# Kernel optimization log

Hardware: AMD Instinct MI355X
Metric: run time of the kernel (lower is better)

Reference implementation:

```python
import jax, jax.numpy as jnp
import numpy as np

NEG = 0.01  # leaky_relu negative slope used throughout AttentiveFP


def _seg_softmax(logits, seg, num):
    # softmax over entries grouped by segment id (PyG softmax w/ 1e-16 eps)
    m = jax.ops.segment_max(logits, seg, num_segments=num)
    m = jnp.where(jnp.isfinite(m), m, 0.0)
    e = jnp.exp(logits - m[seg])
    s = jax.ops.segment_sum(e, seg, num_segments=num)
    return e / (s[seg] + 1e-16)


def _gru(x, h, wi, wh, bi, bh):
    # torch.nn.GRUCell math
    gi = x @ wi.T + bi
    gh = h @ wh.T + bh
    ir, iz, inn = jnp.split(gi, 3, axis=-1)
    hr, hz, hn = jnp.split(gh, 3, axis=-1)
    r = jax.nn.sigmoid(ir + hr)
    z = jax.nn.sigmoid(iz + hz)
    n = jnp.tanh(inn + r * hn)
    return (1.0 - z) * n + z * h


def _forward(x, edge_attr, mol_feats, lin1_w, lin1_b, gate_lin1_w, gate_lin2_w, gate_att_l, gate_att_r, gate_bias, grus_wi, grus_wh, grus_bi, grus_bh, atom_w, atom_att_src, atom_att_dst, atom_bias, mol_w, mol_att_src, mol_att_dst, mol_bias, lin2_w, lin2_b, fcm0_w, fcm0_b, fcm1_w, fcm1_b, fcm2_w, fcm2_b, fc0_w, fc0_b, fc1_w, fc1_b, fc2_w, fc2_b, fc3_w, fc3_b, fc4_w, fc4_b, edge_index, batch):
    N = x.shape[0]
    G = mol_feats.shape[0]
    src, dst = edge_index[0], edge_index[1]
    lrelu = lambda v: jax.nn.leaky_relu(v, NEG)
    # AttentiveFP (eval mode: dropout off)
    xh = lrelu(x @ lin1_w.T + lin1_b)  # [N,H]
    # --- GATEConv: edge-conditioned attention, add aggregation ---
    m = lrelu(jnp.concatenate([xh[src], edge_attr], axis=-1) @ gate_lin1_w.T)  # [E,H]
    a = lrelu(m @ gate_att_l + (xh @ gate_att_r)[dst])
    a = _seg_softmax(a, dst, N)
    h = jax.ops.segment_sum((m @ gate_lin2_w.T) * a[:, None], dst, num_segments=N) + gate_bias
    xh = jax.nn.relu(_gru(jax.nn.elu(h), xh, grus_wi[0], grus_wh[0], grus_bi[0], grus_bh[0]))
    # --- GATConv layers (num_layers-1 = 2, heads=1, no self loops) ---
    for l in range(2):
        xl = xh @ atom_w[l].T
        a = lrelu((xl @ atom_att_src[l])[src] + (xl @ atom_att_dst[l])[dst])
        a = _seg_softmax(a, dst, N)
        h = jax.ops.segment_sum(xl[src] * a[:, None], dst, num_segments=N) + atom_bias[l]
        xh = jax.nn.relu(_gru(jax.nn.elu(h), xh, grus_wi[1 + l], grus_wh[1 + l], grus_bi[1 + l], grus_bh[1 + l]))
    # --- attentive graph readout (num_timesteps = 3) ---
    out = jax.nn.relu(jax.ops.segment_sum(xh, batch, num_segments=G))  # [G,H]
    xm = xh @ mol_w.T            # atom-side lin (x fixed across timesteps)
    a_src = xm @ mol_att_src
    for _ in range(3):
        a = lrelu(a_src + ((out @ mol_w.T) @ mol_att_dst)[batch])
        a = _seg_softmax(a, batch, G)
        h = jax.ops.segment_sum(xm * a[:, None], batch, num_segments=G) + mol_bias
        out = jax.nn.relu(_gru(jax.nn.elu(h), out, grus_wi[3], grus_wh[3], grus_bi[3], grus_bh[3]))
    hg = out @ lin2_w.T + lin2_b  # [G,256]
    # --- mol-feature MLP branch (SiLU) ---
    hm = jax.nn.silu(mol_feats @ fcm0_w.T + fcm0_b)
    hm = jax.nn.silu(hm @ fcm1_w.T + fcm1_b)
    hm = jax.nn.silu(hm @ fcm2_w.T + fcm2_b)
    # --- fusion MLP ---
    hg = jnp.concatenate([hg, hm], axis=1)  # [G,512]
    hg = jax.nn.silu(hg @ fc0_w.T + fc0_b)
    hg = jax.nn.silu(hg @ fc1_w.T + fc1_b)
    hg = jax.nn.silu(hg @ fc2_w.T + fc2_b)
    hg = jax.nn.silu(hg @ fc3_w.T + fc3_b)
    return hg @ fc4_w.T + fc4_b  # [G,1]


def setup_inputs() -> dict:
    key = jax.random.key(0)
    ks = iter(jax.random.split(key, 64))
    def W(*shape):
        return jax.random.normal(next(ks), shape, jnp.float32) / np.float32(np.sqrt(shape[-1]))
    def B(*shape):
        return 0.02 * jax.random.normal(next(ks), shape, jnp.float32)
    N, E, G = 131072, 262144, 8192
    Fn, Fe, Fm, H = 64, 16, 200, 256
    return dict(
        x=jax.random.normal(next(ks), (N, Fn), jnp.float32),
        edge_attr=jax.random.normal(next(ks), (E, Fe), jnp.float32),
        mol_feats=jax.random.normal(next(ks), (G, Fm), jnp.float32),
        lin1_w=W(H, Fn), lin1_b=B(H),
        gate_lin1_w=W(H, H + Fe), gate_lin2_w=W(H, H),
        gate_att_l=W(H), gate_att_r=W(H), gate_bias=B(H),
        grus_wi=W(4, 3 * H, H), grus_wh=W(4, 3 * H, H), grus_bi=B(4, 3 * H), grus_bh=B(4, 3 * H),
        atom_w=W(2, H, H), atom_att_src=W(2, H), atom_att_dst=W(2, H), atom_bias=B(2, H),
        mol_w=W(H, H), mol_att_src=W(H), mol_att_dst=W(H), mol_bias=B(H),
        lin2_w=W(H, H), lin2_b=B(H),
        fcm0_w=W(H, Fm), fcm0_b=B(H), fcm1_w=W(H, H), fcm1_b=B(H), fcm2_w=W(H, H), fcm2_b=B(H),
        fc0_w=W(512, 512), fc0_b=B(512), fc1_w=W(512, 512), fc1_b=B(512),
        fc2_w=W(512, 512), fc2_b=B(512), fc3_w=W(128, 512), fc3_b=B(128),
        fc4_w=W(1, 128), fc4_b=B(1),
        edge_index=jax.random.randint(next(ks), (2, E), 0, N),
        batch=jnp.sort(jax.random.randint(next(ks), (N,), 0, G)),
    )


def reference(x, edge_attr, mol_feats, lin1_w, lin1_b, gate_lin1_w, gate_lin2_w, gate_att_l, gate_att_r, gate_bias, grus_wi, grus_wh, grus_bi, grus_bh, atom_w, atom_att_src, atom_att_dst, atom_bias, mol_w, mol_att_src, mol_att_dst, mol_bias, lin2_w, lin2_b, fcm0_w, fcm0_b, fcm1_w, fcm1_b, fcm2_w, fcm2_b, fc0_w, fc0_b, fc1_w, fc1_b, fc2_w, fc2_b, fc3_w, fc3_b, fc4_w, fc4_b, edge_index, batch):
    return _forward(x, edge_attr, mol_feats, lin1_w, lin1_b, gate_lin1_w, gate_lin2_w, gate_att_l, gate_att_r, gate_bias, grus_wi, grus_wh, grus_bi, grus_bh, atom_w, atom_att_src, atom_att_dst, atom_bias, mol_w, mol_att_src, mol_att_dst, mol_bias, lin2_w, lin2_b, fcm0_w, fcm0_b, fcm1_w, fcm1_b, fcm2_w, fcm2_b, fc0_w, fc0_b, fc1_w, fc1_b, fc2_w, fc2_b, fc3_w, fc3_b, fc4_w, fc4_b, edge_index, batch)
```

## Files before the change

### kernel.cpp

```cpp
#include <hip/hip_runtime.h>
#include <hip/hip_bf16.h>
#include <math.h>


typedef unsigned short u16;
typedef u16 u16x8 __attribute__((ext_vector_type(8)));
typedef short s16x8 __attribute__((ext_vector_type(8)));
typedef float f32x4 __attribute__((ext_vector_type(4)));

__device__ __forceinline__ float u2f(u16 u) { return __uint_as_float(((unsigned)u) << 16); }
__device__ __forceinline__ u16 f2u(float f) {
    return __builtin_bit_cast(u16, __float2bfloat16(f));
}

#define NEGS 0.01f

typedef const __attribute__((address_space(1))) unsigned gas1_t;
typedef __attribute__((address_space(3))) unsigned las3_t;
__device__ __forceinline__ void gload16(const void* g, void* l) {
    __builtin_amdgcn_global_load_lds((gas1_t*)g, (las3_t*)l, 16, 0, 0);
}

__device__ __forceinline__ unsigned fkey(float f) {
    unsigned u = __float_as_uint(f);
    return (u & 0x80000000u) ? ~u : (u | 0x80000000u);
}
__device__ __forceinline__ float funkey(unsigned k) {
    return (k & 0x80000000u) ? __uint_as_float(k ^ 0x80000000u) : __uint_as_float(~k);
}
#define KEY_NEG_INF 0x007FFFFFu

static inline int cdiv(int a, int b) { return (a + b - 1) / b; }

__global__ void fill_f32(float* p, float v, size_t n) {
    size_t i = (size_t)blockIdx.x * 256 + threadIdx.x;
    if (i < n) p[i] = v;
}
__global__ void fill_u32(unsigned* p, unsigned v, int n) {
    int i = blockIdx.x * 256 + threadIdx.x;
    if (i < n) p[i] = v;
}
__global__ void copy_f2b(const float* s, u16* d, size_t n) {
    size_t i = (size_t)blockIdx.x * 256 + threadIdx.x;
    if (i < n) d[i] = f2u(s[i]);
}
__global__ void matvecT_k(const float* W, const float* a, float* v, int K, int Jout) {
    int j = blockIdx.x * 256 + threadIdx.x;
    if (j >= Jout) return;
    float s = 0.f;
    for (int k = 0; k < K; k++) s += W[(size_t)k * Jout + j] * a[k];
    v[j] = s;
}
__global__ void edge_add_lrelu(float* elog, const float* r, const int* dsti, int E) {
    int i = blockIdx.x * 256 + threadIdx.x;
    if (i < E) {
        float v = elog[i] + r[dsti[i]];
        elog[i] = v > 0.f ? v : NEGS * v;
    }
}
__global__ void pair_logit(float* elog, const float* s, const float* d,
                           const int* srci, const int* dsti, int E) {
    int i = blockIdx.x * 256 + threadIdx.x;
    if (i < E) {
        float v = s[srci[i]] + d[dsti[i]];
        elog[i] = v > 0.f ? v : NEGS * v;
    }
}
__global__ void node_logit(float* nlog, const float* asrc, const float* wg,
                           const int* batch, int N) {
    int i = blockIdx.x * 256 + threadIdx.x;
    if (i < N) {
        float v = asrc[i] + wg[batch[i]];
        nlog[i] = v > 0.f ? v : NEGS * v;
    }
}
__global__ void seg_max_k(const float* logit, const int* idx, unsigned* key, int n) {
    int i = blockIdx.x * 256 + threadIdx.x;
    if (i < n) atomicMax(&key[idx[i]], fkey(logit[i]));
}
__global__ void seg_exp_k(const float* logit, const int* idx, const unsigned* key,
                          float* ex, float* sum, int n) {
    int i = blockIdx.x * 256 + threadIdx.x;
    if (i < n) {
        float e = expf(logit[i] - funkey(key[idx[i]]));
        ex[i] = e;
        atomicAdd(&sum[idx[i]], e);
    }
}
__global__ void seg_div_k(const float* ex, const int* idx, const float* sum,
                          float* a, int n) {
    int i = blockIdx.x * 256 + threadIdx.x;
    if (i < n) a[i] = ex[i] / (sum[idx[i]] + 1e-16f);
}
__global__ void rowdot2_b(const u16* X, const float* v1, const float* v2,
                          float* o1, float* o2, int M) {
    int r = blockIdx.x * 4 + (threadIdx.x >> 6);
    int lane = threadIdx.x & 63;
    if (r >= M) return;
    const u16* row = X + (size_t)r * 256 + lane * 4;
    float p1 = 0.f, p2 = 0.f;
#pragma unroll
    for (int q = 0; q < 4; q++) {
        float xv = u2f(row[q]);
        p1 += xv * v1[lane * 4 + q];
        if (v2) p2 += xv * v2[lane * 4 + q];
    }
    for (int off = 32; off; off >>= 1) {
        p1 += __shfl_down(p1, off);
        if (v2) p2 += __shfl_down(p2, off);
    }
    if (lane == 0) {
        o1[r] = p1;
        if (v2) o2[r] = p2;
    }
}
__global__ void rowdot_f(const float* X, const float* v1, float* o1, int M) {
    int r = blockIdx.x * 4 + (threadIdx.x >> 6);
    int lane = threadIdx.x & 63;
    if (r >= M) return;
    float4 a = ((const float4*)(X + (size_t)r * 256))[lane];
    float4 b = ((const float4*)v1)[lane];
    float p1 = a.x * b.x + a.y * b.y + a.z * b.z + a.w * b.w;
    for (int off = 32; off; off >>= 1) p1 += __shfl_down(p1, off);
    if (lane == 0) o1[r] = p1;
}
__global__ void fc4_k(const float* X, const float* w, const float* b, float* out, int G) {
    int g = blockIdx.x * 4 + (threadIdx.x >> 6);
    int lane = threadIdx.x & 63;
    if (g >= G) return;
    float2 xv = ((const float2*)(X + (size_t)g * 128))[lane];
    float2 wv = ((const float2*)w)[lane];
    float p = xv.x * wv.x + xv.y * wv.y;
    for (int off = 32; off; off >>= 1) p += __shfl_down(p, off);
    if (lane == 0) out[g] = p + b[0];
}

__global__ void count_dst(const int* dst, int* cnt, int E) {
    int i = blockIdx.x * 256 + threadIdx.x;
    if (i < E) atomicAdd(&cnt[dst[i]], 1);
}
__global__ void scan1(const int* cnt, int* part, int N) {
    __shared__ int sm[256];
    int i = blockIdx.x * 256 + threadIdx.x;
    sm[threadIdx.x] = i < N ? cnt[i] : 0;
    __syncthreads();
    for (int off = 128; off; off >>= 1) {
        if (threadIdx.x < off) sm[threadIdx.x] += sm[threadIdx.x + off];
        __syncthreads();
    }
    if (threadIdx.x == 0) part[blockIdx.x] = sm[0];
}
__global__ void scan2(int* part, int nb) {
    __shared__ int a[1024], b[1024];
    int t = threadIdx.x;
    if (nb > 1024) {
        if (t == 0) {
            int acc = 0;
            for (int i = 0; i < nb; i++) { int v = part[i]; part[i] = acc; acc += v; }
        }
        return;
    }
    int v = t < nb ? part[t] : 0;
    a[t] = v;
    __syncthreads();
    int* cur = a; int* nxt = b;
    for (int off = 1; off < 1024; off <<= 1) {
        int s = cur[t] + (t >= off ? cur[t - off] : 0);
        nxt[t] = s;
        __syncthreads();
        int* tmp = cur; cur = nxt; nxt = tmp;
    }
    if (t < nb) part[t] = cur[t] - v;
}
__global__ void scan3(const int* cnt, const int* part, int* rowstart, int N) {
    __shared__ int a[256], b[256];
    int t = threadIdx.x;
    int i = blockIdx.x * 256 + t;
    int v = i < N ? cnt[i] : 0;
    a[t] = v;
    __syncthreads();
    int* cur = a; int* nxt = b;
    for (int off = 1; off < 256; off <<= 1) {
        int s = cur[t] + (t >= off ? cur[t - off] : 0);
        nxt[t] = s;
        __syncthreads();
        int* tmp = cur; cur = nxt; nxt = tmp;
    }
    if (i < N) rowstart[i] = part[blockIdx.x] + cur[t] - v;
}
__global__ void fill_csr(const int* dst, const int* rowstart, int* fillc,
                         int* eorder, int* erank, int E) {
    int e = blockIdx.x * 256 + threadIdx.x;
    if (e >= E) return;
    int d = dst[e];
    int s = rowstart[d] + atomicAdd(&fillc[d], 1);
    eorder[s] = e;
    erank[e] = s;
}
__global__ void chunk_dlo_k(const int* rowstart, const int* cnt, int N, int Crows,
                            int nch, int* dlo) {
    int c = blockIdx.x * 64 + threadIdx.x;
    if (c >= nch) return;
    int s0 = c * Crows;
    int lo = 0, hi = N;
    while (lo < hi) {
        int mid = (lo + hi) >> 1;
        if (rowstart[mid] + cnt[mid] > s0) hi = mid; else lo = mid + 1;
    }
    dlo[c] = lo;
}
template <int MODE>
__global__ void csr_red(const int* rowstart, const int* cnt, const int* eorder,
                        const float* a, const int* srcE,
                        const u16* X, const u16* X2, int msplit,
                        int s0, int s1, const int* dlo,
                        u16* outH, u16* outL, int N) {
    int d;
    if (MODE == 1) {
        d = dlo[0] + blockIdx.x;
        if (d >= N) return;
        if (rowstart[d] >= s1) return;
    } else {
        d = blockIdx.x;
        if (d >= N) return;
    }
    int rs = rowstart[d], k = cnt[d];
    int lo = rs, hi = rs + k;
    if (MODE == 1) {
        if (lo < s0) lo = s0;
        if (hi > s1) hi = s1;
        if (lo >= hi) return;
    }
    int c = threadIdx.x;
    float acc = 0.f;
    for (int s = lo; s < hi; s++) {
        int e = eorder[s];
        float av = a[e];
        const u16* row;
        if (MODE == 0) row = X + (size_t)srcE[e] * 256;
        else if (MODE == 1) row = X + (size_t)(s - s0) * 256;
        else row = (s < msplit) ? X + (size_t)s * 256 : X2 + (size_t)(s - msplit) * 256;
        acc += av * u2f(row[c]);
    }
    size_t o = (size_t)d * 256 + c;
    if (MODE == 1) acc += u2f(outH[o]) + u2f(outL[o]);
    u16 hh = f2u(acc);
    outH[o] = hh;
    outL[o] = f2u(acc - u2f(hh));
}
__global__ void graph_bounds(const int* batch, int* gs, int* ge, int N) {
    int i = blockIdx.x * 256 + threadIdx.x;
    if (i >= N) return;
    int b = batch[i];
    atomicMin(&gs[b], i);
    atomicMax(&ge[b], i + 1);
}
template <bool RELU>
__global__ void seg_red(const int* gs, const int* ge, const u16* X, const float* sc,
                        float* out, int G) {
    int g = blockIdx.x;
    if (g >= G) return;
    int c = threadIdx.x;
    int s = gs[g], e = ge[g];
    float acc = 0.f;
    if (s < e)
        for (int i = s; i < e; i++) {
            float v = u2f(X[(size_t)i * 256 + c]);
            if (sc) v *= sc[i];
            acc += v;
        }
    out[(size_t)g * 256 + c] = RELU ? fmaxf(acc, 0.f) : acc;
}

__global__ void pack_w(const float* s1, const float* s2, int K1, int Ksrc,
                       int Nout, int Kp, u16* dst) {
    int idx = blockIdx.x * 256 + threadIdx.x;
    int kiters = Kp >> 5;
    int total = (Nout >> 7) * kiters * 512;
    if (idx >= total) return;
    int c = idx & 511;
    int rest = idx >> 9;
    int ki = rest % kiters, nb = rest / kiters;
    int n = (nb << 7) + (((c >> 6) & 7) << 4) + (c & 15);
    int k0 = (ki << 5) + (((c >> 4) & 3) << 3);
    u16x8 vh, vl;
#pragma unroll
    for (int j = 0; j < 8; j++) {
        int k = k0 + j;
        float f = 0.f;
        if (k < K1) f = s1[(size_t)n * K1 + k];
        else if (k < Ksrc) f = s2[(size_t)n * (Ksrc - K1) + (k - K1)];
        u16 h = f2u(f);
        vh[j] = h;
        vl[j] = f2u(f - u2f(h));
    }
    ((u16x8*)dst)[idx] = vh;
    ((u16x8*)dst)[idx + total] = vl;
}
__global__ void pack_gru_w(const float* wi, const float* wh, u16* dst) {
    int idx = blockIdx.x * 256 + threadIdx.x;
    const int total = 8 * 16 * 512;
    if (idx >= total) return;
    int c = idx & 511, rest = idx >> 9;
    int ki = rest & 15, nb = rest >> 4;
    int n = (nb << 7) + (((c >> 6) & 7) << 4) + (c & 15);
    int k0 = (ki << 5) + (((c >> 4) & 3) << 3);
    int grp = n >> 6, sub = (n >> 4) & 3, ch = grp * 16 + (n & 15);
    u16x8 vh, vl;
#pragma unroll
    for (int j = 0; j < 8; j++) {
        int k = k0 + j;
        float f;
        if (sub < 3) {
            int srow = sub * 256 + ch;
            f = (k < 256) ? wi[(size_t)srow * 256 + k]
                          : wh[(size_t)srow * 256 + (k - 256)];
        } else {
            f = (k < 256) ? 0.f : wh[(size_t)(512 + ch) * 256 + (k - 256)];
        }
        u16 h = f2u(f);
        vh[j] = h;
        vl[j] = f2u(f - u2f(h));
    }
    ((u16x8*)dst)[idx] = vh;
    ((u16x8*)dst)[idx + total] = vl;
}
__global__ void pack_gru_b(const float* bi, const float* bh, float* bp) {
    int n = blockIdx.x * 256 + threadIdx.x;
    if (n >= 1024) return;
    int grp = n >> 6, sub = (n >> 4) & 3, ch = grp * 16 + (n & 15);
    float v;
    if (sub == 0) v = bi[ch] + bh[ch];
    else if (sub == 1) v = bi[256 + ch] + bh[256 + ch];
    else if (sub == 2) v = bi[512 + ch] + bh[512 + ch];
    else v = bh[512 + ch];
    bp[n] = v;
}

struct p8 { u16x8 hi, lo; };
__device__ __forceinline__ u16x8 zero8() {
    u16x8 z;
#pragma unroll
    for (int j = 0; j < 8; j++) z[j] = 0;
    return z;
}
__device__ __forceinline__ p8 sp_zero() { p8 r; r.hi = zero8(); r.lo = zero8(); return r; }
__device__ __forceinline__ p8 sp_b(const u16* p) {
    p8 r;
    r.hi = *(const u16x8*)p;
    r.lo = zero8();
    return r;
}
__device__ __forceinline__ p8 sp_f(const float* p) {
    p8 r;
#pragma unroll
    for (int j = 0; j < 8; j++) {
        float x = p[j];
        u16 h = f2u(x);
        r.hi[j] = h;
        r.lo[j] = f2u(x - u2f(h));
    }
    return r;
}
__device__ __forceinline__ p8 sp_eluf(const float* p) {
    p8 r;
#pragma unroll
    for (int j = 0; j < 8; j++) {
        float x = p[j];
        float e = x > 0.f ? x : expm1f(x);
        u16 h = f2u(e);
        r.hi[j] = h;
        r.lo[j] = f2u(e - u2f(h));
    }
    return r;
}
template <int ALD>
__device__ __forceinline__ p8 ldA(bool valid, int k, int Ksrc, const u16* ab,
                                  const float* af, const float* x2) {
    if (!valid) return sp_zero();
    if (ALD == 1) {
        if (k >= Ksrc) return sp_zero();
        return sp_f(af + k);
    }
    if (ALD == 2 || ALD == 7) {
        if (k < 256) return sp_b(ab + k);
        if (k < 272) return sp_f(x2 + (k - 256));
        return sp_zero();
    }
    if (k < 256) return sp_eluf(af + k);
    return sp_f(x2 + (k - 256));
}
template <int ALD>
__device__ __forceinline__ bool lo_zero(int ki) {
    if (ALD == 2 || ALD == 7) return ki < 8;
    return false;
}
template <int ACT>
__device__ __forceinline__ float actf(float v) {
    if (ACT == 1) return v > 0.f ? v : NEGS * v;
    if (ACT == 3) return v / (1.f + expf(-v));
    return v;
}

template <int ALD, int ACT, int EPI>
__global__ __launch_bounds__(256, 4) void mgemm(
    int M, int Kp, int Ksrc,
    const float* Af, int lda, const u16* Ab, const u16* Ab2,
    const int* gidx, const float* X2f, const u16* Wp, const float* b1,
    float* Cf, u16* Cb, u16* Cb2, int csplit, int ldc,
    const float* attv, float* dotout, const int* didx) {
    __shared__ u16x8 lsAh[512];
    __shared__ u16x8 lsAl[512];
    const int t = threadIdx.x;
    const int m0 = blockIdx.x * 128;
    const int nb = blockIdx.y;
    const int kiters = Kp >> 5;
    const int r0 = ((t >> 6) << 4) | (t & 15);
    const int kq = ((t >> 4) & 3) << 3;
    const int mA[2] = {m0 + r0, m0 + r0 + 64};
    const u16* abh[2]; const u16* abl[2];
    const float* afr[2]; const float* x2r[2];
    bool val[2];
#pragma unroll
    for (int h = 0; h < 2; h++) {
        int m = mA[h];
        val[h] = (m < M);
        int ms = val[h] ? m : 0;
        abh[h] = nullptr; abl[h] = nullptr; afr[h] = nullptr; x2r[h] = nullptr;
        if constexpr (ALD == 1) {
            afr[h] = Af + (size_t)ms * lda;
        } else if constexpr (ALD == 2) {
            abh[h] = Ab + (size_t)gidx[ms] * 256;
            x2r[h] = X2f + (size_t)ms * 16;
        } else if constexpr (ALD == 7) {
            int e = gidx[ms];
            abh[h] = Ab + (size_t)didx[e] * 256;
            x2r[h] = X2f + (size_t)e * 16;
        } else {
            abh[h] = Ab + (size_t)ms * 256;
            abl[h] = Ab2 + (size_t)ms * 256;
        }
    }
    const int wave = t >> 6, lane = t & 63;
    const int wm = (wave >> 1) << 6, wn = (wave & 1) << 6;
    f32x4 acc[4][4];
#pragma unroll
    for (int i = 0; i < 4; i++)
#pragma unroll
        for (int j = 0; j < 4; j++) {
            acc[i][j][0] = 0.f; acc[i][j][1] = 0.f; acc[i][j][2] = 0.f; acc[i][j][3] = 0.f;
        }
    const u16x8* wh0 = (const u16x8*)Wp + ((size_t)nb * kiters << 9);
    const u16x8* wl0 = wh0 + ((size_t)gridDim.y * kiters << 9);
    const int wfrag = (wn >> 4) * 64 + lane;
    for (int ki = 0; ki < kiters; ki++) {
        int kb = (ki << 5) + kq;
        if constexpr (ALD == 6) {
            gload16(abh[0] + kb, &lsAh[t]);
            gload16(abh[1] + kb, &lsAh[t + 256]);
            gload16(abl[0] + kb, &lsAl[t]);
            gload16(abl[1] + kb, &lsAl[t + 256]);
        } else {
            p8 a0 = ldA<ALD>(val[0], kb, Ksrc, abh[0], afr[0], x2r[0]);
            p8 a1 = ldA<ALD>(val[1], kb, Ksrc, abh[1], afr[1], x2r[1]);
            lsAh[t] = a0.hi; lsAl[t] = a0.lo;
            lsAh[t + 256] = a1.hi; lsAl[t + 256] = a1.lo;
        }
        __syncthreads();
        bool skip_lh = lo_zero<ALD>(ki);
        s16x8 ah[4], al[4];
#pragma unroll
        for (int f = 0; f < 4; f++) {
            int ai = ((wm >> 4) + f) * 64 + lane;
            ah[f] = __builtin_bit_cast(s16x8, lsAh[ai]);
        }
        if (!skip_lh) {
#pragma unroll
            for (int f = 0; f < 4; f++) {
                int ai = ((wm >> 4) + f) * 64 + lane;
                al[f] = __builtin_bit_cast(s16x8, lsAl[ai]);
            }
        }
        const u16x8* wsh = wh0 + ((size_t)ki << 9) + wfrag;
        const u16x8* wsl = wl0 + ((size_t)ki << 9) + wfrag;
#pragma unroll
        for (int fj = 0; fj < 4; fj++) {
            s16x8 wh = __builtin_bit_cast(s16x8, wsh[fj * 64]);
            s16x8 wl = __builtin_bit_cast(s16x8, wsl[fj * 64]);
#pragma unroll
            for (int fi = 0; fi < 4; fi++) {
                acc[fi][fj] = __builtin_amdgcn_mfma_f32_16x16x32_bf16(
                    ah[fi], wh, acc[fi][fj], 0, 0, 0);
                if (!skip_lh)
                    acc[fi][fj] = __builtin_amdgcn_mfma_f32_16x16x32_bf16(
                        al[fi], wh, acc[fi][fj], 0, 0, 0);
                acc[fi][fj] = __builtin_amdgcn_mfma_f32_16x16x32_bf16(
                    ah[fi], wl, acc[fi][fj], 0, 0, 0);
            }
        }
        __syncthreads();
    }
    const int col = lane & 15, quad = lane >> 4;
    const int n_base = nb * 128 + wn;
    if constexpr (EPI == 2) {
        float dp[4][4] = {};
#pragma unroll
        for (int fi = 0; fi < 4; fi++)
#pragma unroll
            for (int fj = 0; fj < 4; fj++) {
                int nn = n_base + fj * 16 + col;
                float av = attv[nn];
#pragma unroll
                for (int r = 0; r < 4; r++) {
                    float v = actf<ACT>(acc[fi][fj][r]);
                    dp[fi][r] += v * av;
                    if (Cb) {
                        int mm = m0 + wm + fi * 16 + quad * 4 + r;
                        if (mm < M) {
                            int s = didx[mm];
                            u16* bb_ = (s < csplit) ? Cb : Cb2;
                            size_t ro = (s < csplit) ? (size_t)s * 256
                                                     : (size_t)(s - csplit) * 256;
                            bb_[ro + nn] = f2u(v);
                        }
                    }
                }
            }
#pragma unroll
        for (int fi = 0; fi < 4; fi++)
#pragma unroll
            for (int r = 0; r < 4; r++) {
                float p = dp[fi][r];
                p += __shfl_down(p, 8);
                p += __shfl_down(p, 4);
                p += __shfl_down(p, 2);
                p += __shfl_down(p, 1);
                int mm = m0 + wm + fi * 16 + quad * 4 + r;
                if (col == 0 && mm < M) atomicAdd(dotout + mm, p);
            }
    } else if constexpr (EPI == 4) {
#pragma unroll
        for (int fj = 0; fj < 4; fj++) {
            int nn = n_base + fj * 16 + col;
            float bb = b1 ? b1[nn] : 0.f;
#pragma unroll
            for (int fi = 0; fi < 4; fi++)
#pragma unroll
                for (int r = 0; r < 4; r++) {
                    int mm = m0 + wm + fi * 16 + quad * 4 + r;
                    if (mm >= M) continue;
                    float v = acc[fi][fj][r] + bb;
                    float e = v > 0.f ? v : expm1f(v);
                    u16 hh = f2u(e);
                    size_t o = (size_t)mm * ldc + nn;
                    Cb[o] = hh;
                    Cb2[o] = f2u(e - u2f(hh));
                }
        }
    } else {
#pragma unroll
        for (int fj = 0; fj < 4; fj++) {
            int nn = n_base + fj * 16 + col;
            float bb = b1 ? b1[nn] : 0.f;
#pragma unroll
            for (int fi = 0; fi < 4; fi++)
#pragma unroll
                for (int r = 0; r < 4; r++) {
                    int mm = m0 + wm + fi * 16 + quad * 4 + r;
                    if (mm >= M) continue;
                    float v = actf<ACT>(acc[fi][fj][r] + bb);
                    if (EPI == 1) Cb[(size_t)mm * ldc + nn] = f2u(v);
                    else Cf[(size_t)mm * ldc + nn] = v;
                }
        }
    }
}

template <int ALD, bool HB, bool OB>
__global__ __launch_bounds__(256, 4) void mgemm_gru(
    int M, const float* Af, const u16* Ab, const u16* Ab2, const float* X2f,
    const u16* Wp, const float* bp, const u16* hb, const float* hf,
    float* of, u16* ob) {
    __shared__ u16x8 lsAh[512];
    __shared__ u16x8 lsAl[512];
    const int t = threadIdx.x;
    const int m0 = blockIdx.x * 128;
    const int nb = blockIdx.y;
    const int r0 = ((t >> 6) << 4) | (t & 15);
    const int kq = ((t >> 4) & 3) << 3;
    const int mA[2] = {m0 + r0, m0 + r0 + 64};
    const u16* ehr[2]; const u16* elr[2]; const u16* xhr[2];
    const float* afr[2]; const float* x2r[2];
    bool val[2];
#pragma unroll
    for (int h = 0; h < 2; h++) {
        int m = mA[h];
        val[h] = (m < M);
        int ms = val[h] ? m : 0;
        ehr[h] = nullptr; elr[h] = nullptr; xhr[h] = nullptr;
        afr[h] = nullptr; x2r[h] = nullptr;
        if constexpr (ALD == 5) {
            ehr[h] = Ab + (size_t)ms * 256;
            elr[h] = Ab2 + (size_t)ms * 256;
            xhr[h] = hb + (size_t)ms * 256;
        } else {
            afr[h] = Af + (size_t)ms * 256;
            x2r[h] = X2f + (size_t)ms * 256;
        }
    }
    const int wave = t >> 6, lane = t & 63;
    const int wm = (wave >> 1) << 6, wn = (wave & 1) << 6;
    f32x4 acc[4][4];
#pragma unroll
    for (int i = 0; i < 4; i++)
#pragma unroll
        for (int j = 0; j < 4; j++) {
            acc[i][j][0] = 0.f; acc[i][j][1] = 0.f; acc[i][j][2] = 0.f; acc[i][j][3] = 0.f;
        }
    const u16x8* wh0 = (const u16x8*)Wp + ((size_t)nb * 16 << 9);
    const u16x8* wl0 = (const u16x8*)Wp + (size_t)(8 * 16 * 512) + ((size_t)nb * 16 << 9);
    const int wfrag = (wn >> 4) * 64 + lane;
    for (int ki = 0; ki < 16; ki++) {
        int kb = (ki << 5) + kq;
        if constexpr (ALD == 5) {
            const u16* p0 = kb < 256 ? ehr[0] + kb : xhr[0] + (kb - 256);
            const u16* p1 = kb < 256 ? ehr[1] + kb : xhr[1] + (kb - 256);
            gload16(p0, &lsAh[t]);
            gload16(p1, &lsAh[t + 256]);
            if (ki < 8) {
                gload16(elr[0] + kb, &lsAl[t]);
                gload16(elr[1] + kb, &lsAl[t + 256]);
            }
        } else {
            p8 a0 = ldA<4>(val[0], kb, 512, nullptr, afr[0], x2r[0]);
            p8 a1 = ldA<4>(val[1], kb, 512, nullptr, afr[1], x2r[1]);
            lsAh[t] = a0.hi; lsAl[t] = a0.lo;
            lsAh[t + 256] = a1.hi; lsAl[t + 256] = a1.lo;
        }
        __syncthreads();
        bool skip_lh = (ALD == 5) ? (ki >= 8) : false;
        bool hn_zero = (ki < 8);
        s16x8 ah[4], al[4];
#pragma unroll
        for (int f = 0; f < 4; f++) {
            int ai = ((wm >> 4) + f) * 64 + lane;
            ah[f] = __builtin_bit_cast(s16x8, lsAh[ai]);
        }
        if (!skip_lh) {
#pragma unroll
            for (int f = 0; f < 4; f++) {
                int ai = ((wm >> 4) + f) * 64 + lane;
                al[f] = __builtin_bit_cast(s16x8, lsAl[ai]);
            }
        }
        const u16x8* wsh = wh0 + ((size_t)ki << 9) + wfrag;
        const u16x8* wsl = wl0 + ((size_t)ki << 9) + wfrag;
#pragma unroll
        for (int fj = 0; fj < 4; fj++) {
            if (fj == 3 && hn_zero) continue;
            s16x8 wh = __builtin_bit_cast(s16x8, wsh[fj * 64]);
            s16x8 wl = __builtin_bit_cast(s16x8, wsl[fj * 64]);
#pragma unroll
            for (int fi = 0; fi < 4; fi++) {
                acc[fi][fj] = __builtin_amdgcn_mfma_f32_16x16x32_bf16(
                    ah[fi], wh, acc[fi][fj], 0, 0, 0);
                if (!skip_lh)
                    acc[fi][fj] = __builtin_amdgcn_mfma_f32_16x16x32_bf16(
                        al[fi], wh, acc[fi][fj], 0, 0, 0);
                acc[fi][fj] = __builtin_amdgcn_mfma_f32_16x16x32_bf16(
                    ah[fi], wl, acc[fi][fj], 0, 0, 0);
            }
        }
        __syncthreads();
    }
    const int col = lane & 15, quad = lane >> 4;
    const int nbase = nb * 128 + wn;
    float br = bp[nbase + col];
    float bz = bp[nbase + 16 + col];
    float bn = bp[nbase + 32 + col];
    float bhn = bp[nbase + 48 + col];
    int ch = (nb * 2 + (wn >> 6)) * 16 + col;
#pragma unroll
    for (int fi = 0; fi < 4; fi++)
#pragma unroll
        for (int r = 0; r < 4; r++) {
            int m = m0 + wm + fi * 16 + quad * 4 + r;
            if (m >= M) continue;
            float rs = acc[fi][0][r] + br;
            float zs = acc[fi][1][r] + bz;
            float nsv = acc[fi][2][r] + bn;
            float hnv = acc[fi][3][r] + bhn;
            float rr = 1.f / (1.f + expf(-rs));
            float zz = 1.f / (1.f + expf(-zs));
            float nn = tanhf(nsv - hnv + rr * hnv);
            float ho = HB ? u2f(hb[(size_t)m * 256 + ch]) : hf[(size_t)m * 256 + ch];
            float o = fmaxf((1.f - zz) * nn + zz * ho, 0.f);
            if (OB) ob[(size_t)m * 256 + ch] = f2u(o);
            else of[(size_t)m * 256 + ch] = o;
        }
}

extern "C" void kernel_launch(void* const* d_in, const int* in_sizes, int n_in,
                              void* d_out, int out_size, void* d_ws, size_t ws_size,
                              hipStream_t stream) {
    const float* x = (const float*)d_in[0];
    const float* edge_attr = (const float*)d_in[1];
    const float* mol_feats = (const float*)d_in[2];
    const float* lin1_w = (const float*)d_in[3];
    const float* lin1_b = (const float*)d_in[4];
    const float* gate_lin1_w = (const float*)d_in[5];
    const float* gate_lin2_w = (const float*)d_in[6];
    const float* gate_att_l = (const float*)d_in[7];
    const float* gate_att_r = (const float*)d_in[8];
    const float* gate_bias = (const float*)d_in[9];
    const float* grus_wi = (const float*)d_in[10];
    const float* grus_wh = (const float*)d_in[11];
    const float* grus_bi = (const float*)d_in[12];
    const float* grus_bh = (const float*)d_in[13];
    const float* atom_w = (const float*)d_in[14];
    const float* atom_att_src = (const float*)d_in[15];
    const float* atom_att_dst = (const float*)d_in[16];
    const float* atom_bias = (const float*)d_in[17];
    const float* mol_w = (const float*)d_in[18];
    const float* mol_att_src = (const float*)d_in[19];
    const float* mol_att_dst = (const float*)d_in[20];
    const float* mol_bias = (const float*)d_in[21];
    const float* lin2_w = (const float*)d_in[22];
    const float* lin2_b = (const float*)d_in[23];
    const float* fcm0_w = (const float*)d_in[24];
    const float* fcm0_b = (const float*)d_in[25];
    const float* fcm1_w = (const float*)d_in[26];
    const float* fcm1_b = (const float*)d_in[27];
    const float* fcm2_w = (const float*)d_in[28];
    const float* fcm2_b = (const float*)d_in[29];
    const float* fc0_w = (const float*)d_in[30];
    const float* fc0_b = (const float*)d_in[31];
    const float* fc1_w = (const float*)d_in[32];
    const float* fc1_b = (const float*)d_in[33];
    const float* fc2_w = (const float*)d_in[34];
    const float* fc2_b = (const float*)d_in[35];
    const float* fc3_w = (const float*)d_in[36];
    const float* fc3_b = (const float*)d_in[37];
    const float* fc4_w = (const float*)d_in[38];
    const float* fc4_b = (const float*)d_in[39];
    const int* edge_index = (const int*)d_in[40];
    const int* batch = (const int*)d_in[41];
    float* out_final = (float*)d_out;

    const int N = in_sizes[0] / 64;
    const int E = in_sizes[1] / 16;
    const int G = in_sizes[2] / 200;
    const int* srcE = edge_index;
    const int* dstE = edge_index + E;

    char* base = (char*)d_ws;
    size_t off = 0;
    auto alloc = [&](size_t bytes) -> char* {
        char* p = base + off;
        off += (bytes + 255) & ~(size_t)255;
        return p;
    };
    u16* xhA = (u16*)alloc((size_t)N * 512);
    u16* haggH = (u16*)alloc((size_t)N * 512);
    u16* haggL = (u16*)alloc((size_t)N * 512);
    float* outg = (float*)alloc((size_t)G * 1024);
    float* hgrb = (float*)alloc((size_t)G * 1024);
    float* elog = (float*)alloc((size_t)E * 4);
    float* eexp = (float*)alloc((size_t)E * 4);
    float* aedge = (float*)alloc((size_t)E * 4);
    unsigned* nkey = (unsigned*)alloc((size_t)N * 4);
    float* nsum = (float*)alloc((size_t)N * 4);
    float* ns1 = (float*)alloc((size_t)N * 4);
    float* ns2 = (float*)alloc((size_t)N * 4);
    unsigned* gkey = (unsigned*)alloc((size_t)G * 4);
    float* gsum = (float*)alloc((size_t)G * 4);
    float* wgb = (float*)alloc((size_t)G * 4);
    float* vbuf = (float*)alloc(4096);
    int* ecnt = (int*)alloc((size_t)N * 4);
    int* efill = (int*)alloc((size_t)N * 4);
    int* erowst = (int*)alloc((size_t)N * 4);
    int* eorder = (int*)alloc((size_t)E * 4);
    int* erank = (int*)alloc((size_t)E * 4);
    int* spart = (int*)alloc(4096 * 4);
    int* cdlo = (int*)alloc(((size_t)E / 128 + 2) * 4);
    int* gs = (int*)alloc((size_t)G * 4);
    int* ge = (int*)alloc((size_t)G * 4);
    u16* pk_lin1 = (u16*)alloc(256 * 64 * 2 * 2);
    u16* pk_g1 = (u16*)alloc(256 * 288 * 2 * 2);
    u16* pk_g2 = (u16*)alloc(256 * 256 * 2 * 2);
    u16* pk_gruF[4];
    float* bp_gru[4];
    for (int l = 0; l < 4; l++) {
        pk_gruF[l] = (u16*)alloc(1024 * 512 * 2 * 2);
        bp_gru[l] = (float*)alloc(1024 * 4);
    }
    u16* pk_atom[2];
    for (int l = 0; l < 2; l++) pk_atom[l] = (u16*)alloc(256 * 256 * 2 * 2);
    u16* pk_mol = (u16*)alloc(256 * 256 * 2 * 2);
    u16* pk_lin2 = (u16*)alloc(256 * 256 * 2 * 2);
    u16* pk_fcm0 = (u16*)alloc(256 * 224 * 2 * 2);
    u16* pk_fcm1 = (u16*)alloc(256 * 256 * 2 * 2);
    u16* pk_fcm2 = (u16*)alloc(256 * 256 * 2 * 2);
    u16* pk_fc0 = (u16*)alloc(512 * 512 * 2 * 2);
    u16* pk_fc1 = (u16*)alloc(512 * 512 * 2 * 2);
    u16* pk_fc2 = (u16*)alloc(512 * 512 * 2 * 2);
    u16* pk_fc3 = (u16*)alloc(128 * 512 * 2 * 2);
    size_t fixed_core = off;
    if (fixed_core + (size_t)2 * 1024 * 1024 > ws_size) {
        fill_f32<<<cdiv(out_size, 256), 256, 0, stream>>>(out_final, (float)ws_size,
                                                          (size_t)out_size);
        return;
    }
    u16* xhB = nullptr;
    bool use_pp = false;
    if (ws_size - off >= (size_t)N * 512 + (size_t)2 * 1024 * 1024) {
        xhB = (u16*)alloc((size_t)N * 512);
        use_pp = true;
    }
    size_t workbytes = ws_size - off;
    char* workp = base + off;
    int Mc = (int)((workbytes / (use_pp ? 1024 : 2048)) & ~(size_t)127);
    if (Mc > N) Mc = N;
    if (Mc < 128) Mc = 128;
    u16* ehi = (u16*)workp;
    u16* elo = ehi + (size_t)Mc * 256;
    float* htmp = (float*)(workp + (size_t)Mc * 1024);
    float* cbuf = (float*)workp;
    u16* mt1 = nullptr; u16* mt2 = nullptr; int msplit = 0x7fffffff;
    if (workbytes >= (size_t)E * 512) { mt1 = (u16*)workp; msplit = E; }
    else if (use_pp) {
        if (N >= E) { mt1 = xhB; msplit = E; }
        else if ((size_t)N * 512 + workbytes >= (size_t)E * 512) {
            mt1 = xhB; msplit = N; mt2 = (u16*)workp;
        }
    }
    bool gate_store = (mt1 != nullptr);
    size_t crows_sz = workbytes / 512;
    if (crows_sz > (size_t)E) crows_sz = (size_t)E;
    int Crows = (int)(crows_sz & ~(size_t)127);
    if (Crows < 128) Crows = 128;
    int nch = cdiv(E, Crows);
    u16* mchunk = (u16*)workp;
    float* fbufA = (float*)haggH;
    float* fbufB = fbufA + (size_t)G * 512;
    float* fbufC = fbufB + (size_t)G * 512;
    float* f128 = fbufC + (size_t)G * 512;
    float* hm1 = f128 + (size_t)G * 128;
    float* hm2 = hm1 + (size_t)G * 256;

    auto pack = [&](const float* s1, const float* s2, int K1, int Ksrc, int Nout,
                    int Kp, u16* dst) {
        int total = (Nout >> 7) * (Kp >> 5) * 512;
        pack_w<<<cdiv(total, 256), 256, 0, stream>>>(s1, s2, K1, Ksrc, Nout, Kp, dst);
    };
    pack(lin1_w, nullptr, 64, 64, 256, 64, pk_lin1);
    pack(gate_lin1_w, nullptr, 272, 272, 256, 288, pk_g1);
    pack(gate_lin2_w, nullptr, 256, 256, 256, 256, pk_g2);
    for (int l = 0; l < 4; l++) {
        pack_gru_w<<<cdiv(8 * 16 * 512, 256), 256, 0, stream>>>(
            grus_wi + (size_t)l * 768 * 256, grus_wh + (size_t)l * 768 * 256,
            pk_gruF[l]);
        pack_gru_b<<<4, 256, 0, stream>>>(grus_bi + (size_t)l * 768,
                                          grus_bh + (size_t)l * 768, bp_gru[l]);
    }
    for (int l = 0; l < 2; l++)
        pack(atom_w + (size_t)l * 256 * 256, nullptr, 256, 256, 256, 256, pk_atom[l]);
    pack(mol_w, nullptr, 256, 256, 256, 256, pk_mol);
    pack(lin2_w, nullptr, 256, 256, 256, 256, pk_lin2);
    pack(fcm0_w, nullptr, 200, 200, 256, 224, pk_fcm0);
    pack(fcm1_w, nullptr, 256, 256, 256, 256, pk_fcm1);
    pack(fcm2_w, nullptr, 256, 256, 256, 256, pk_fcm2);
    pack(fc0_w, nullptr, 512, 512, 512, 512, pk_fc0);
    pack(fc1_w, nullptr, 512, 512, 512, 512, pk_fc1);
    pack(fc2_w, nullptr, 512, 512, 512, 512, pk_fc2);
    pack(fc3_w, nullptr, 512, 512, 128, 512, pk_fc3);

    int nbk = cdiv(N, 256);
    fill_u32<<<nbk, 256, 0, stream>>>((unsigned*)ecnt, 0u, N);
    fill_u32<<<nbk, 256, 0, stream>>>((unsigned*)efill, 0u, N);
    count_dst<<<cdiv(E, 256), 256, 0, stream>>>(dstE, ecnt, E);
    scan1<<<nbk, 256, 0, stream>>>(ecnt, spart, N);
    scan2<<<1, 1024, 0, stream>>>(spart, nbk);
    scan3<<<nbk, 256, 0, stream>>>(ecnt, spart, erowst, N);
    fill_csr<<<cdiv(E, 256), 256, 0, stream>>>(dstE, erowst, efill, eorder, erank, E);
    fill_u32<<<cdiv(G, 256), 256, 0, stream>>>((unsigned*)gs, (unsigned)N, G);
    fill_u32<<<cdiv(G, 256), 256, 0, stream>>>((unsigned*)ge, 0u, G);
    graph_bounds<<<nbk, 256, 0, stream>>>(batch, gs, ge, N);

    u16* xh_cur = xhA;
    u16* xh_nxt = xhB;

    auto node_gru = [&](int l, const u16* Wpre, const float* bpre) {
        for (int c0 = 0; c0 < N; c0 += Mc) {
            int Ms = N - c0 < Mc ? N - c0 : Mc;
            int gx = cdiv(Ms, 128);
            mgemm<6, 0, 4><<<dim3(gx, 2), 256, 0, stream>>>(Ms, 256, 256,
                nullptr, 0, haggH + (size_t)c0 * 256, haggL + (size_t)c0 * 256,
                nullptr, nullptr, Wpre, bpre,
                nullptr, ehi, elo, 0, 256, nullptr, nullptr, nullptr);
            if (use_pp) {
                mgemm_gru<5, true, true><<<dim3(gx, 8), 256, 0, stream>>>(Ms,
                    nullptr, ehi, elo, nullptr, pk_gruF[l], bp_gru[l],
                    xh_cur + (size_t)c0 * 256, nullptr,
                    nullptr, xh_nxt + (size_t)c0 * 256);
            } else {
                mgemm_gru<5, true, false><<<dim3(gx, 8), 256, 0, stream>>>(Ms,
                    nullptr, ehi, elo, nullptr, pk_gruF[l], bp_gru[l],
                    xh_cur + (size_t)c0 * 256, nullptr,
                    htmp, nullptr);
                copy_f2b<<<(int)(((size_t)Ms * 256 + 255) / 256), 256, 0, stream>>>(
                    htmp, xh_cur + (size_t)c0 * 256, (size_t)Ms * 256);
            }
        }
        if (use_pp) { u16* t2 = xh_cur; xh_cur = xh_nxt; xh_nxt = t2; }
    };

    mgemm<1, 1, 1><<<dim3(cdiv(N, 128), 2), 256, 0, stream>>>(N, 64, 64,
        x, 64, nullptr, nullptr, nullptr, nullptr, pk_lin1, lin1_b,
        nullptr, xh_cur, nullptr, 0, 256, nullptr, nullptr, nullptr);

    fill_f32<<<cdiv(E, 256), 256, 0, stream>>>(elog, 0.f, (size_t)E);
    mgemm<2, 1, 2><<<dim3(cdiv(E, 128), 2), 256, 0, stream>>>(E, 288, 272,
        nullptr, 0, xh_cur, nullptr, srcE, edge_attr, pk_g1, nullptr,
        nullptr, gate_store ? mt1 : nullptr, mt2, msplit, 256,
        gate_att_l, elog, erank);
    rowdot2_b<<<cdiv(N, 4), 256, 0, stream>>>(xh_cur, gate_att_r, nullptr, ns1, nullptr, N);
    edge_add_lrelu<<<cdiv(E, 256), 256, 0, stream>>>(elog, ns1, dstE, E);
    fill_u32<<<nbk, 256, 0, stream>>>(nkey, KEY_NEG_INF, N);
    fill_f32<<<nbk, 256, 0, stream>>>(nsum, 0.f, (size_t)N);
    seg_max_k<<<cdiv(E, 256), 256, 0, stream>>>(elog, dstE, nkey, E);
    seg_exp_k<<<cdiv(E, 256), 256, 0, stream>>>(elog, dstE, nkey, eexp, nsum, E);
    seg_div_k<<<cdiv(E, 256), 256, 0, stream>>>(eexp, dstE, nsum, aedge, E);
    if (gate_store) {
        csr_red<2><<<N, 256, 0, stream>>>(erowst, ecnt, eorder, aedge, nullptr,
            mt1, mt2, msplit, 0, E, nullptr, haggH, haggL, N);
    } else {
        fill_u32<<<cdiv(N * 256, 256), 256, 0, stream>>>((unsigned*)haggH, 0u, N * 256);
        chunk_dlo_k<<<cdiv(nch, 64), 64, 0, stream>>>(erowst, ecnt, N, Crows, nch, cdlo);
        for (int c = 0; c < nch; c++) {
            int s0 = c * Crows;
            int s1 = s0 + Crows < E ? s0 + Crows : E;
            int Ms = s1 - s0;
            mgemm<7, 1, 1><<<dim3(cdiv(Ms, 128), 2), 256, 0, stream>>>(Ms, 288, 272,
                nullptr, 0, xh_cur, nullptr, eorder + s0, edge_attr, pk_g1, nullptr,
                nullptr, mchunk, nullptr, 0x7fffffff, 256,
                nullptr, nullptr, srcE);
            csr_red<1><<<Crows, 256, 0, stream>>>(erowst, ecnt, eorder, aedge, nullptr,
                mchunk, nullptr, 0, s0, s1, cdlo + c, haggH, haggL, N);
        }
    }
    node_gru(0, pk_g2, gate_bias);

    for (int l = 0; l < 2; l++) {
        const float* aw = atom_w + (size_t)l * 256 * 256;
        matvecT_k<<<1, 256, 0, stream>>>(aw, atom_att_src + (size_t)l * 256, vbuf, 256, 256);
        matvecT_k<<<1, 256, 0, stream>>>(aw, atom_att_dst + (size_t)l * 256, vbuf + 256, 256, 256);
        rowdot2_b<<<cdiv(N, 4), 256, 0, stream>>>(xh_cur, vbuf, vbuf + 256, ns1, ns2, N);
        pair_logit<<<cdiv(E, 256), 256, 0, stream>>>(elog, ns1, ns2, srcE, dstE, E);
        fill_u32<<<nbk, 256, 0, stream>>>(nkey, KEY_NEG_INF, N);
        fill_f32<<<nbk, 256, 0, stream>>>(nsum, 0.f, (size_t)N);
        seg_max_k<<<cdiv(E, 256), 256, 0, stream>>>(elog, dstE, nkey, E);
        seg_exp_k<<<cdiv(E, 256), 256, 0, stream>>>(elog, dstE, nkey, eexp, nsum, E);
        seg_div_k<<<cdiv(E, 256), 256, 0, stream>>>(eexp, dstE, nsum, aedge, E);
        csr_red<0><<<N, 256, 0, stream>>>(erowst, ecnt, eorder, aedge, srcE,
            xh_cur, nullptr, 0, 0, 0, nullptr, haggH, haggL, N);
        node_gru(1 + l, pk_atom[l], atom_bias + (size_t)l * 256);
    }

    seg_red<true><<<G, 256, 0, stream>>>(gs, ge, xh_cur, nullptr, outg, G);
    matvecT_k<<<1, 256, 0, stream>>>(mol_w, mol_att_dst, vbuf, 256, 256);
    matvecT_k<<<1, 256, 0, stream>>>(mol_w, mol_att_src, vbuf + 256, 256, 256);
    rowdot2_b<<<cdiv(N, 4), 256, 0, stream>>>(xh_cur, vbuf + 256, nullptr, ns1, nullptr, N);
    float* ogc = outg;
    float* ogn = hgrb;
    int McG = Mc < G ? Mc : G;
    for (int t = 0; t < 3; t++) {
        rowdot_f<<<cdiv(G, 4), 256, 0, stream>>>(ogc, vbuf, wgb, G);
        node_logit<<<nbk, 256, 0, stream>>>(elog, ns1, wgb, batch, N);
        fill_u32<<<cdiv(G, 256), 256, 0, stream>>>(gkey, KEY_NEG_INF, G);
        fill_f32<<<cdiv(G, 256), 256, 0, stream>>>(gsum, 0.f, (size_t)G);
        seg_max_k<<<nbk, 256, 0, stream>>>(elog, batch, gkey, N);
        seg_exp_k<<<nbk, 256, 0, stream>>>(elog, batch, gkey, eexp, gsum, N);
        seg_div_k<<<nbk, 256, 0, stream>>>(eexp, batch, gsum, aedge, N);
        seg_red<false><<<G, 256, 0, stream>>>(gs, ge, xh_cur, aedge, ogn, G);
        for (int c0 = 0; c0 < G; c0 += McG) {
            int Ms = G - c0 < McG ? G - c0 : McG;
            int gx = cdiv(Ms, 128);
            mgemm<1, 0, 0><<<dim3(gx, 2), 256, 0, stream>>>(Ms, 256, 256,
                ogn + (size_t)c0 * 256, 256, nullptr, nullptr, nullptr, nullptr,
                pk_mol, mol_bias, cbuf, nullptr, nullptr, 0, 256,
                nullptr, nullptr, nullptr);
            mgemm_gru<4, false, false><<<dim3(gx, 8), 256, 0, stream>>>(Ms,
                cbuf, nullptr, nullptr, ogc + (size_t)c0 * 256, pk_gruF[3], bp_gru[3],
                nullptr, ogc + (size_t)c0 * 256, ogn + (size_t)c0 * 256, nullptr);
        }
        float* tt = ogc; ogc = ogn; ogn = tt;
    }

    int gG = cdiv(G, 128);
    mgemm<1, 0, 0><<<dim3(gG, 2), 256, 0, stream>>>(G, 256, 256, ogc, 256,
        nullptr, nullptr, nullptr, nullptr, pk_lin2, lin2_b,
        fbufA, nullptr, nullptr, 0, 512, nullptr, nullptr, nullptr);
    mgemm<1, 3, 0><<<dim3(gG, 2), 256, 0, stream>>>(G, 224, 200, mol_feats, 200,
        nullptr, nullptr, nullptr, nullptr, pk_fcm0, fcm0_b,
        hm1, nullptr, nullptr, 0, 256, nullptr, nullptr, nullptr);
    mgemm<1, 3, 0><<<dim3(gG, 2), 256, 0, stream>>>(G, 256, 256, hm1, 256,
        nullptr, nullptr, nullptr, nullptr, pk_fcm1, fcm1_b,
        hm2, nullptr, nullptr, 0, 256, nullptr, nullptr, nullptr);
    mgemm<1, 3, 0><<<dim3(gG, 2), 256, 0, stream>>>(G, 256, 256, hm2, 256,
        nullptr, nullptr, nullptr, nullptr, pk_fcm2, fcm2_b,
        fbufA + 256, nullptr, nullptr, 0, 512, nullptr, nullptr, nullptr);
    mgemm<1, 3, 0><<<dim3(gG, 4), 256, 0, stream>>>(G, 512, 512, fbufA, 512,
        nullptr, nullptr, nullptr, nullptr, pk_fc0, fc0_b,
        fbufB, nullptr, nullptr, 0, 512, nullptr, nullptr, nullptr);
    mgemm<1, 3, 0><<<dim3(gG, 4), 256, 0, stream>>>(G, 512, 512, fbufB, 512,
        nullptr, nullptr, nullptr, nullptr, pk_fc1, fc1_b,
        fbufC, nullptr, nullptr, 0, 512, nullptr, nullptr, nullptr);
    mgemm<1, 3, 0><<<dim3(gG, 4), 256, 0, stream>>>(G, 512, 512, fbufC, 512,
        nullptr, nullptr, nullptr, nullptr, pk_fc2, fc2_b,
        fbufB, nullptr, nullptr, 0, 512, nullptr, nullptr, nullptr);
    mgemm<1, 3, 0><<<dim3(gG, 1), 256, 0, stream>>>(G, 512, 512, fbufB, 512,
        nullptr, nullptr, nullptr, nullptr, pk_fc3, fc3_b,
        f128, nullptr, nullptr, 0, 128, nullptr, nullptr, nullptr);
    fc4_k<<<cdiv(G, 4), 256, 0, stream>>>(f128, fc4_w, fc4_b, out_final, G);
}
```

Measured before the change: 6.200 ms.

## Register-prefetch next K-step weight fragments in both MFMA GEMM kernels

Both split-bf16 MFMA GEMM kernels now hold the current K-step's weight fragments in registers and load the next step's fragments from global memory before the current step's MFMAs run. This is meant to hide global-load latency on the weight operand. The extra registers lower the launch-bounds occupancy hint from 4 to 3 blocks per CU. In mgemm the low-half A fragments are also no longer written to LDS when they are known to be zero.

After: 5.979 ms. 1.04x faster.

```diff
diff --git a/kernel.cpp b/kernel.cpp
--- a/kernel.cpp
+++ b/kernel.cpp
@@ -403,7 +403,7 @@
 }
 
 template <int ALD, int ACT, int EPI>
-__global__ __launch_bounds__(256, 4) void mgemm(
+__global__ __launch_bounds__(256, 3) void mgemm(
     int M, int Kp, int Ksrc,
     const float* Af, int lda, const u16* Ab, const u16* Ab2,
     const int* gidx, const float* X2f, const u16* Wp, const float* b1,
@@ -452,9 +452,16 @@
         }
     const u16x8* wh0 = (const u16x8*)Wp + ((size_t)nb * kiters << 9);
     const u16x8* wl0 = wh0 + ((size_t)gridDim.y * kiters << 9);
-    const int wfrag = (wn >> 4) * 64 + lane;
+    const int wbase = ((wn >> 4) << 6) + lane;
+    s16x8 cwh[4], cwl[4];
+#pragma unroll
+    for (int f = 0; f < 4; f++) {
+        cwh[f] = __builtin_bit_cast(s16x8, wh0[wbase + f * 64]);
+        cwl[f] = __builtin_bit_cast(s16x8, wl0[wbase + f * 64]);
+    }
     for (int ki = 0; ki < kiters; ki++) {
         int kb = (ki << 5) + kq;
+        bool skip_lh = lo_zero<ALD>(ki);
         if constexpr (ALD == 6) {
             gload16(abh[0] + kb, &lsAh[t]);
             gload16(abh[1] + kb, &lsAh[t + 256]);
@@ -463,11 +470,23 @@
         } else {
             p8 a0 = ldA<ALD>(val[0], kb, Ksrc, abh[0], afr[0], x2r[0]);
             p8 a1 = ldA<ALD>(val[1], kb, Ksrc, abh[1], afr[1], x2r[1]);
-            lsAh[t] = a0.hi; lsAl[t] = a0.lo;
-            lsAh[t + 256] = a1.hi; lsAl[t + 256] = a1.lo;
+            lsAh[t] = a0.hi;
+            lsAh[t + 256] = a1.hi;
+            if (!skip_lh) {
+                lsAl[t] = a0.lo;
+                lsAl[t + 256] = a1.lo;
+            }
         }
         __syncthreads();
-        bool skip_lh = lo_zero<ALD>(ki);
+        int kn = (ki + 1 < kiters) ? ki + 1 : ki;
+        const u16x8* wshn = wh0 + ((size_t)kn << 9) + wbase;
+        const u16x8* wsln = wl0 + ((size_t)kn << 9) + wbase;
+        s16x8 nwh[4], nwl[4];
+#pragma unroll
+        for (int f = 0; f < 4; f++) {
+            nwh[f] = __builtin_bit_cast(s16x8, wshn[f * 64]);
+            nwl[f] = __builtin_bit_cast(s16x8, wsln[f * 64]);
+        }
         s16x8 ah[4], al[4];
 #pragma unroll
         for (int f = 0; f < 4; f++) {
@@ -481,24 +500,21 @@
                 al[f] = __builtin_bit_cast(s16x8, lsAl[ai]);
             }
         }
-        const u16x8* wsh = wh0 + ((size_t)ki << 9) + wfrag;
-        const u16x8* wsl = wl0 + ((size_t)ki << 9) + wfrag;
-#pragma unroll
-        for (int fj = 0; fj < 4; fj++) {
-            s16x8 wh = __builtin_bit_cast(s16x8, wsh[fj * 64]);
-            s16x8 wl = __builtin_bit_cast(s16x8, wsl[fj * 64]);
-#pragma unroll
-            for (int fi = 0; fi < 4; fi++) {
+#pragma unroll
+        for (int fi = 0; fi < 4; fi++)
+#pragma unroll
+            for (int fj = 0; fj < 4; fj++) {
                 acc[fi][fj] = __builtin_amdgcn_mfma_f32_16x16x32_bf16(
-                    ah[fi], wh, acc[fi][fj], 0, 0, 0);
+                    ah[fi], cwh[fj], acc[fi][fj], 0, 0, 0);
                 if (!skip_lh)
                     acc[fi][fj] = __builtin_amdgcn_mfma_f32_16x16x32_bf16(
-                        al[fi], wh, acc[fi][fj], 0, 0, 0);
+                        al[fi], cwh[fj], acc[fi][fj], 0, 0, 0);
                 acc[fi][fj] = __builtin_amdgcn_mfma_f32_16x16x32_bf16(
-                    ah[fi], wl, acc[fi][fj], 0, 0, 0);
+                    ah[fi], cwl[fj], acc[fi][fj], 0, 0, 0);
             }
-        }
         __syncthreads();
+#pragma unroll
+        for (int f = 0; f < 4; f++) { cwh[f] = nwh[f]; cwl[f] = nwl[f]; }
     }
     const int col = lane & 15, quad = lane >> 4;
     const int n_base = nb * 128 + wn;
@@ -577,7 +593,7 @@
 }
 
 template <int ALD, bool HB, bool OB>
-__global__ __launch_bounds__(256, 4) void mgemm_gru(
+__global__ __launch_bounds__(256, 3) void mgemm_gru(
     int M, const float* Af, const u16* Ab, const u16* Ab2, const float* X2f,
     const u16* Wp, const float* bp, const u16* hb, const float* hf,
     float* of, u16* ob) {
@@ -619,9 +635,17 @@
         }
     const u16x8* wh0 = (const u16x8*)Wp + ((size_t)nb * 16 << 9);
     const u16x8* wl0 = (const u16x8*)Wp + (size_t)(8 * 16 * 512) + ((size_t)nb * 16 << 9);
-    const int wfrag = (wn >> 4) * 64 + lane;
+    const int wbase = ((wn >> 4) << 6) + lane;
+    s16x8 cwh[4], cwl[4];
+#pragma unroll
+    for (int f = 0; f < 4; f++) {
+        cwh[f] = __builtin_bit_cast(s16x8, wh0[wbase + f * 64]);
+        cwl[f] = __builtin_bit_cast(s16x8, wl0[wbase + f * 64]);
+    }
     for (int ki = 0; ki < 16; ki++) {
         int kb = (ki << 5) + kq;
+        bool skip_lh = (ALD == 5) ? (ki >= 8) : false;
+        bool hn_zero = (ki < 8);
         if constexpr (ALD == 5) {
             const u16* p0 = kb < 256 ? ehr[0] + kb : xhr[0] + (kb - 256);
             const u16* p1 = kb < 256 ? ehr[1] + kb : xhr[1] + (kb - 256);
@@ -638,8 +662,15 @@
             lsAh[t + 256] = a1.hi; lsAl[t + 256] = a1.lo;
         }
         __syncthreads();
-        bool skip_lh = (ALD == 5) ? (ki >= 8) : false;
-        bool hn_zero = (ki < 8);
+        int kn = (ki + 1 < 16) ? ki + 1 : ki;
+        const u16x8* wshn = wh0 + ((size_t)kn << 9) + wbase;
+        const u16x8* wsln = wl0 + ((size_t)kn << 9) + wbase;
+        s16x8 nwh[4], nwl[4];
+#pragma unroll
+        for (int f = 0; f < 4; f++) {
+            nwh[f] = __builtin_bit_cast(s16x8, wshn[f * 64]);
+            nwl[f] = __builtin_bit_cast(s16x8, wsln[f * 64]);
+        }
         s16x8 ah[4], al[4];
 #pragma unroll
         for (int f = 0; f < 4; f++) {
@@ -653,25 +684,22 @@
                 al[f] = __builtin_bit_cast(s16x8, lsAl[ai]);
             }
         }
-        const u16x8* wsh = wh0 + ((size_t)ki << 9) + wfrag;
-        const u16x8* wsl = wl0 + ((size_t)ki << 9) + wfrag;
-#pragma unroll
-        for (int fj = 0; fj < 4; fj++) {
-            if (fj == 3 && hn_zero) continue;
-            s16x8 wh = __builtin_bit_cast(s16x8, wsh[fj * 64]);
-            s16x8 wl = __builtin_bit_cast(s16x8, wsl[fj * 64]);
-#pragma unroll
-            for (int fi = 0; fi < 4; fi++) {
+#pragma unroll
+        for (int fi = 0; fi < 4; fi++)
+#pragma unroll
+            for (int fj = 0; fj < 4; fj++) {
+                if (fj == 3 && hn_zero) continue;
                 acc[fi][fj] = __builtin_amdgcn_mfma_f32_16x16x32_bf16(
-                    ah[fi], wh, acc[fi][fj], 0, 0, 0);
+                    ah[fi], cwh[fj], acc[fi][fj], 0, 0, 0);
                 if (!skip_lh)
                     acc[fi][fj] = __builtin_amdgcn_mfma_f32_16x16x32_bf16(
-                        al[fi], wh, acc[fi][fj], 0, 0, 0);
+                        al[fi], cwh[fj], acc[fi][fj], 0, 0, 0);
                 acc[fi][fj] = __builtin_amdgcn_mfma_f32_16x16x32_bf16(
-                    ah[fi], wl, acc[fi][fj], 0, 0, 0);
+                    ah[fi], cwl[fj], acc[fi][fj], 0, 0, 0);
             }
-        }
         __syncthreads();
+#pragma unroll
+        for (int f = 0; f < 4; f++) { cwh[f] = nwh[f]; cwl[f] = nwl[f]; }
     }
     const int col = lane & 15, quad = lane >> 4;
     const int nbase = nb * 128 + wn;
```
